# Performance work log

Measured on AMD Instinct MI355X. Metric: run time of the kernel, lower is better.

Reference implementation:

```python
import jax, jax.numpy as jnp
import numpy as np

D_MODEL = 1024
HEADS = 16
HEAD_DIM = D_MODEL // HEADS


def setup_inputs() -> dict:
    key = jax.random.key(0)
    k1, k2 = jax.random.split(key)
    x = jax.random.normal(k1, (2, 2048, D_MODEL), dtype=jnp.float32)
    # nn.Linear(d_model, 3*d_model, bias=False): weight shape [3*d_model, d_model]
    W_qkv = jax.random.normal(k2, (3 * D_MODEL, D_MODEL), dtype=jnp.float32) * (D_MODEL ** -0.5)
    return {"x": x, "W_qkv": W_qkv}


def reference(x, W_qkv):
    b, t, c = x.shape
    qkv = jnp.einsum('btc,fc->btf', x, W_qkv)  # [b, t, 3c]
    q, k, v = jnp.split(qkv, 3, axis=-1)
    # [b, heads, t, head_dim]
    q = q.reshape(b, t, HEADS, HEAD_DIM).transpose(0, 2, 1, 3)
    k = k.reshape(b, t, HEADS, HEAD_DIM).transpose(0, 2, 1, 3)
    v = v.reshape(b, t, HEADS, HEAD_DIM).transpose(0, 2, 1, 3)
    scores = jnp.einsum('bhqd,bhkd->bhqk', q, k) * (HEAD_DIM ** -0.5)
    causal = jnp.tril(jnp.ones((t, t), dtype=bool))  # [t, t]
    scores = jnp.where(causal[None, None, :, :], scores, -jnp.inf)
    weights = jax.nn.softmax(scores, axis=-1)
    out = jnp.einsum('bhqk,bhkd->bhqd', weights, v)
    return out.transpose(0, 2, 1, 3).reshape(b, t, c)
```

## Files before the change

kernel.cpp:

```cpp
#include <hip/hip_runtime.h>
#include <hip/hip_bf16.h>
#include <stdint.h>

#define D_MODEL 1024
#define TOKENS  2048
#define HEADS   16
#define HDIM    64
#define NQKV    3072
#define MROWS   4096
#define SCALE   0.18033688011112042f

typedef __attribute__((ext_vector_type(4)))  float f32x4;
typedef __attribute__((ext_vector_type(16))) float f32x16;
typedef __attribute__((ext_vector_type(8)))  short bf16x8;

__device__ __forceinline__ unsigned short f2bf(float f) {
  union { float f; unsigned u; } v; v.f = f;
  unsigned u = v.u + 0x7FFFu + ((v.u >> 16) & 1u);
  return (unsigned short)(u >> 16);
}
__device__ __forceinline__ float bf2f(unsigned short b) {
  union { unsigned u; float f; } v; v.u = ((unsigned)b) << 16;
  return v.f;
}
__device__ __forceinline__ unsigned cvt_pk_bf16(float lo, float hi) {
  unsigned r;
  asm("v_cvt_pk_bf16_f32 %0, %1, %2" : "=v"(r) : "v"(lo), "v"(hi));
  return r;
}
__device__ __forceinline__ float xchg32(float v) {
  return __shfl_xor(v, 32);
}
__device__ __forceinline__ bf16x8 pfrag8(const float* g) {
  union { uint4 u; bf16x8 v; } r;
  r.u.x = cvt_pk_bf16(g[0], g[1]);
  r.u.y = cvt_pk_bf16(g[2], g[3]);
  r.u.z = cvt_pk_bf16(g[4], g[5]);
  r.u.w = cvt_pk_bf16(g[6], g[7]);
  return r.v;
}
__device__ __forceinline__ float max32t(const f32x16& a, const f32x16& b) {
  float t[16];
#pragma unroll
  for (int r = 0; r < 16; ++r) t[r] = fmaxf(a[r], b[r]);
#pragma unroll
  for (int s = 8; s > 0; s >>= 1)
#pragma unroll
    for (int r = 0; r < s; ++r) t[r] = fmaxf(t[r], t[r + s]);
  return t[0];
}
__device__ __forceinline__ float sum32t(const float* a, const float* b) {
  float t[16];
#pragma unroll
  for (int r = 0; r < 16; ++r) t[r] = a[r] + b[r];
#pragma unroll
  for (int s = 8; s > 0; s >>= 1)
#pragma unroll
    for (int r = 0; r < s; ++r) t[r] = t[r] + t[r + s];
  return t[0];
}

#define GLOAD16(g, l)                                                          \
  __builtin_amdgcn_global_load_lds(                                            \
      (const __attribute__((address_space(1))) unsigned int*)(g),              \
      (__attribute__((address_space(3))) unsigned int*)(l), 16, 0, 0)

__global__ __launch_bounds__(256) void cvt_bf16(const float* __restrict__ X,
                                                const float* __restrict__ W,
                                                unsigned short* __restrict__ Xb,
                                                unsigned short* __restrict__ Wb) {
  const size_t NX = (size_t)MROWS * D_MODEL;
  size_t i = ((size_t)blockIdx.x * 256 + threadIdx.x) * 8;
  const float* src; unsigned short* dst; size_t off;
  if (i < NX) { src = X; dst = Xb; off = i; }
  else        { src = W; dst = Wb; off = i - NX; }
  float4 a = ((const float4*)(src + off))[0];
  float4 b = ((const float4*)(src + off))[1];
  union { unsigned short s[8]; uint4 v; } u;
  u.s[0] = f2bf(a.x); u.s[1] = f2bf(a.y); u.s[2] = f2bf(a.z); u.s[3] = f2bf(a.w);
  u.s[4] = f2bf(b.x); u.s[5] = f2bf(b.y); u.s[6] = f2bf(b.z); u.s[7] = f2bf(b.w);
  *(uint4*)(dst + off) = u.v;
}

__global__ __launch_bounds__(512, 1) void gemm8(const unsigned short* __restrict__ A,
                                                const unsigned short* __restrict__ B,
                                                unsigned short* __restrict__ C) {
  __shared__ unsigned short sA[2][2][128][64];
  __shared__ unsigned short sB[2][2][128][64];

  const int tid  = threadIdx.x;
  const int lane = tid & 63;
  const int wave = tid >> 6;
  const int wr   = wave >> 2;
  const int wc   = wave & 3;
  const int l15  = lane & 15;
  const int lg   = lane >> 4;

  const int bm = blockIdx.x;
  const int bn = blockIdx.y;

  f32x4 acc[8][4];
#pragma unroll
  for (int i = 0; i < 8; ++i)
#pragma unroll
    for (int j = 0; j < 4; ++j)
#pragma unroll
      for (int r = 0; r < 4; ++r) acc[i][j][r] = 0.f;

  const int srow = tid >> 3;
  const int scb  = (tid & 7) * 16;
  const int ssce = (scb ^ ((srow & 7) << 4)) >> 1;

  const unsigned short* Ag = A + (size_t)(bm * 256) * D_MODEL;
  const unsigned short* Bg = B + (size_t)(bn * 256) * D_MODEL;

#define STG_A(buf, hf, t)                                                      \
  { GLOAD16(Ag + (size_t)((hf) * 128 + srow) * D_MODEL + (t) * 64 + ssce,      \
            (char*)&sA[buf][hf][0][0] + srow * 128 + scb);                     \
    GLOAD16(Ag + (size_t)((hf) * 128 + 64 + srow) * D_MODEL + (t) * 64 + ssce, \
            (char*)&sA[buf][hf][0][0] + 8192 + srow * 128 + scb); }
#define STG_B(buf, hf, t)                                                      \
  { GLOAD16(Bg + (size_t)((hf) * 128 + srow) * D_MODEL + (t) * 64 + ssce,      \
            (char*)&sB[buf][hf][0][0] + srow * 128 + scb);                     \
    GLOAD16(Bg + (size_t)((hf) * 128 + 64 + srow) * D_MODEL + (t) * 64 + ssce, \
            (char*)&sB[buf][hf][0][0] + 8192 + srow * 128 + scb); }

  const char* aBse[2] = { (const char*)&sA[0][wr][0][0], (const char*)&sA[1][wr][0][0] };
  const char* bBse[2] = { (const char*)&sB[0][wc >> 1][0][0], (const char*)&sB[1][wc >> 1][0][0] };
  const int swzl = (l15 & 7) << 4;
  const int cbs0 = (lg * 16) ^ swzl;
  const int cbs1 = (64 + lg * 16) ^ swzl;
  const int arow = l15 * 128;
  const int brow = ((wc & 1) * 64 + l15) * 128;

  bf16x8 aF[4][2];

#define DO_PHASE(qm, qn, buf, LD_A, STAGE_STMT, DO_VM)                         \
  {                                                                            \
    if (LD_A) {                                                                \
      _Pragma("unroll")                                                        \
      for (int i = 0; i < 4; ++i) {                                            \
        aF[i][0] = *(const bf16x8*)(aBse[buf] + ((qm)*4 + i) * 2048 + arow + cbs0); \
        aF[i][1] = *(const bf16x8*)(aBse[buf] + ((qm)*4 + i) * 2048 + arow + cbs1); \
      }                                                                        \
    }                                                                          \
    bf16x8 b_[2][2];                                                           \
    _Pragma("unroll")                                                          \
    for (int n = 0; n < 2; ++n) {                                              \
      b_[n][0] = *(const bf16x8*)(bBse[buf] + ((qn)*2 + n) * 2048 + brow + cbs0); \
      b_[n][1] = *(const bf16x8*)(bBse[buf] + ((qn)*2 + n) * 2048 + brow + cbs1); \
    }                                                                          \
    STAGE_STMT;                                                                \
    if (DO_VM) asm volatile("s_waitcnt vmcnt(2)" ::: "memory");                \
    __builtin_amdgcn_s_barrier();                                              \
    asm volatile("s_waitcnt lgkmcnt(0)" ::: "memory");                         \
    __builtin_amdgcn_sched_barrier(0);                                         \
    __builtin_amdgcn_s_setprio(1);                                             \
    _Pragma("unroll")                                                          \
    for (int ks = 0; ks < 2; ++ks)                                             \
      _Pragma("unroll")                                                        \
      for (int i = 0; i < 4; ++i)                                              \
        _Pragma("unroll")                                                      \
        for (int n = 0; n < 2; ++n)                                            \
          acc[(qm)*4 + i][(qn)*2 + n] = __builtin_amdgcn_mfma_f32_16x16x32_bf16( \
              aF[i][ks], b_[n][ks], acc[(qm)*4 + i][(qn)*2 + n], 0, 0, 0);     \
    __builtin_amdgcn_s_setprio(0);                                             \
    __builtin_amdgcn_s_barrier();                                              \
  }

  STG_A(0, 0, 0);
  STG_B(0, 0, 0);
  STG_A(0, 1, 0);
  STG_B(0, 1, 0);
  STG_B(1, 0, 1);
  asm volatile("s_waitcnt vmcnt(2)" ::: "memory");
  __builtin_amdgcn_s_barrier();

#pragma unroll 1
  for (int j = 0; j < 8; ++j) {
    const int t1 = 2 * j + 1;
    const int t2 = 2 * j + 2;
    const int t3 = 2 * j + 3;
    DO_PHASE(0, 0, 0, 1, { STG_A(1, 0, t1); }, 0);
    DO_PHASE(0, 1, 0, 0, { STG_A(1, 1, t1); }, 0);
    DO_PHASE(1, 0, 0, 1, { STG_B(1, 1, t1); }, 0);
    DO_PHASE(1, 1, 0, 0, { if (t2 < 16) STG_B(0, 0, t2); }, 1);
    DO_PHASE(0, 0, 1, 1, { if (t2 < 16) STG_A(0, 0, t2); }, 0);
    DO_PHASE(0, 1, 1, 0, { if (t2 < 16) STG_A(0, 1, t2); }, 0);
    DO_PHASE(1, 0, 1, 1, { if (t2 < 16) STG_B(0, 1, t2); }, 0);
    DO_PHASE(1, 1, 1, 0, { if (t3 < 16) STG_B(1, 0, t3); }, 1);
  }

  const int orow0 = bm * 256 + wr * 128 + lg * 4;
  const int ocol0 = bn * 256 + wc * 64 + l15;
#pragma unroll
  for (int mi = 0; mi < 8; ++mi)
#pragma unroll
    for (int ni = 0; ni < 4; ++ni)
#pragma unroll
      for (int r = 0; r < 4; ++r)
        C[(size_t)(orow0 + mi * 16 + r) * NQKV + ocol0 + ni * 16] = f2bf(acc[mi][ni][r]);
#undef STG_A
#undef STG_B
#undef DO_PHASE
}

__global__ __launch_bounds__(256) void qkv_gemm(const float* __restrict__ X,
                                                const float* __restrict__ W,
                                                unsigned short* __restrict__ QKV) {
  __shared__ unsigned short sA[128 * 32];
  __shared__ unsigned short sB[128 * 32];
  const int tid  = threadIdx.x;
  const int lane = tid & 63;
  const int wave = tid >> 6;
  const int wr = wave >> 1, wc = wave & 1;
  const int row0 = blockIdx.x * 128;
  const int col0 = blockIdx.y * 128;

  f32x4 acc[4][4];
#pragma unroll
  for (int i = 0; i < 4; ++i)
#pragma unroll
    for (int j = 0; j < 4; ++j)
#pragma unroll
      for (int r = 0; r < 4; ++r) acc[i][j][r] = 0.f;

  const int srow = tid >> 1;
  const int scol = (tid & 1) * 16;
  union U16 { unsigned short s[8]; uint4 v; };

#pragma unroll 1
  for (int k0 = 0; k0 < D_MODEL; k0 += 32) {
    {
      const float* ga = X + (size_t)(row0 + srow) * D_MODEL + k0 + scol;
      const float* gb = W + (size_t)(col0 + srow) * D_MODEL + k0 + scol;
      float va[16], vb[16];
#pragma unroll
      for (int i = 0; i < 4; ++i) {
        float4 t = ((const float4*)ga)[i];
        va[4*i+0] = t.x; va[4*i+1] = t.y; va[4*i+2] = t.z; va[4*i+3] = t.w;
        float4 u = ((const float4*)gb)[i];
        vb[4*i+0] = u.x; vb[4*i+1] = u.y; vb[4*i+2] = u.z; vb[4*i+3] = u.w;
      }
      U16 ua0, ua1, ub0, ub1;
#pragma unroll
      for (int e = 0; e < 8; ++e) {
        ua0.s[e] = f2bf(va[e]);   ua1.s[e] = f2bf(va[8 + e]);
        ub0.s[e] = f2bf(vb[e]);   ub1.s[e] = f2bf(vb[8 + e]);
      }
      *(uint4*)&sA[srow * 32 + scol + 0] = ua0.v;
      *(uint4*)&sA[srow * 32 + scol + 8] = ua1.v;
      *(uint4*)&sB[srow * 32 + scol + 0] = ub0.v;
      *(uint4*)&sB[srow * 32 + scol + 8] = ub1.v;
    }
    __syncthreads();

    const int lrow = lane & 15;
    const int lk   = (lane >> 4) * 8;
    bf16x8 av[4], bv[4];
#pragma unroll
    for (int i = 0; i < 4; ++i)
      av[i] = *(const bf16x8*)&sA[(wr * 64 + i * 16 + lrow) * 32 + lk];
#pragma unroll
    for (int j = 0; j < 4; ++j)
      bv[j] = *(const bf16x8*)&sB[(wc * 64 + j * 16 + lrow) * 32 + lk];
#pragma unroll
    for (int i = 0; i < 4; ++i)
#pragma unroll
      for (int j = 0; j < 4; ++j)
        acc[i][j] = __builtin_amdgcn_mfma_f32_16x16x32_bf16(av[i], bv[j], acc[i][j], 0, 0, 0);
    __syncthreads();
  }

  const int orow = row0 + wr * 64 + (lane >> 4) * 4;
  const int ocol = col0 + wc * 64 + (lane & 15);
#pragma unroll
  for (int i = 0; i < 4; ++i)
#pragma unroll
    for (int j = 0; j < 4; ++j)
#pragma unroll
      for (int r = 0; r < 4; ++r)
        QKV[(size_t)(orow + i * 16 + r) * NQKV + ocol + j * 16] = f2bf(acc[i][j][r]);
}

__global__ __launch_bounds__(256, 2) void attn10(const unsigned short* __restrict__ QKV,
                                                 float* __restrict__ Out) {
  __shared__ unsigned short sK [2][2][64 * 64];
  __shared__ unsigned short sVt[2][2][64 * 64];

  const int tid  = threadIdx.x;
  const int lane = tid & 63;
  const int wave = tid >> 6;
  const int l31  = lane & 31;
  const int hi   = lane >> 5;

  const int x = blockIdx.x;
  int bh, u;
  if (x < 256) { bh = x & 31; u = x >> 5; }
  else         { const int x2 = x - 256; bh = x2 & 31; u = 15 - (x2 >> 5); }

  const int b = bh >> 4, h = bh & 15;
  const int q0w  = u * 128 + wave * 32;
  const int qcol = q0w + l31;

  const unsigned short* Qbase = QKV + (size_t)(b * TOKENS) * NQKV + h * HDIM;
  const unsigned short* Kbase = Qbase + D_MODEL;
  const unsigned short* Vbase = Kbase + D_MODEL;

  bf16x8 qf[4];
  {
    const unsigned short* qrow = Qbase + (size_t)qcol * NQKV + hi * 8;
    union { unsigned short us[8]; bf16x8 v; ushort4 q[2]; } t;
#pragma unroll
    for (int dk = 0; dk < 4; ++dk) {
      t.q[0] = ((const ushort4*)(qrow + dk * 16))[0];
      t.q[1] = ((const ushort4*)(qrow + dk * 16))[1];
#pragma unroll
      for (int e = 0; e < 8; ++e) t.us[e] = f2bf(bf2f(t.us[e]) * SCALE);
      qf[dk] = t.v;
    }
  }

  f32x16 o0, o1;
#pragma unroll
  for (int r = 0; r < 16; ++r) { o0[r] = 0.f; o1[r] = 0.f; }
  float m = -1e30f, ll = 0.f;

  const int vk0 = (tid & 15) * 4;
  const int vd0 = (tid >> 4) * 4;
  ushort4 va0, va1, va2, va3, vb0, vb1, vb2, vb3;

  const int lane16 = lane * 16;

#define KGLOAD(kt, buf, s)                                                     \
  {                                                                            \
    _Pragma("unroll")                                                          \
    for (int g = 0; g < 2; ++g) {                                              \
      const int base = g * 4096 + wave * 1024;                                 \
      const int d = base + lane16;                                             \
      const int row = d >> 7;                                                  \
      const int grow = (row & 51) | ((row & 4) << 1) | ((row & 8) >> 1);       \
      const int cb = (d & 127) ^ ((row & 7) << 4);                             \
      GLOAD16(Kbase + (size_t)((kt) * 64 + grow) * NQKV + (cb >> 1),           \
              (char*)&sK[buf][s][0] + base + lane16);                          \
    }                                                                          \
  }

#define VLOAD2(pp)                                                             \
  {                                                                            \
    const unsigned short* vsA = Vbase + (size_t)((2*(pp)) * 64 + vk0) * NQKV + vd0;   \
    va0 = *(const ushort4*)(vsA);                                              \
    va1 = *(const ushort4*)(vsA + NQKV);                                       \
    va2 = *(const ushort4*)(vsA + 2 * NQKV);                                   \
    va3 = *(const ushort4*)(vsA + 3 * NQKV);                                   \
    const unsigned short* vsB = Vbase + (size_t)((2*(pp)+1) * 64 + vk0) * NQKV + vd0; \
    vb0 = *(const ushort4*)(vsB);                                              \
    vb1 = *(const ushort4*)(vsB + NQKV);                                       \
    vb2 = *(const ushort4*)(vsB + 2 * NQKV);                                   \
    vb3 = *(const ushort4*)(vsB + 3 * NQKV);                                   \
  }

#define VWRITE1(buf, s, t0, t1, t2, t3)                                        \
  {                                                                            \
    ushort4 c0, c1, c2, c3;                                                    \
    c0.x = t0.x; c0.y = t1.x; c0.z = t2.x; c0.w = t3.x;                        \
    c1.x = t0.y; c1.y = t1.y; c1.z = t2.y; c1.w = t3.y;                        \
    c2.x = t0.z; c2.y = t1.z; c2.z = t2.z; c2.w = t3.z;                        \
    c3.x = t0.w; c3.y = t1.w; c3.z = t2.w; c3.w = t3.w;                        \
    char* dV = (char*)&sVt[buf][s][0];                                         \
    _Pragma("unroll")                                                          \
    for (int e = 0; e < 4; ++e) {                                              \
      const int dim = vd0 + e;                                                 \
      const int o2 = (dim * 128 + vk0 * 2) ^ ((dim & 7) << 4);                 \
      ushort4 cc = (e == 0) ? c0 : (e == 1) ? c1 : (e == 2) ? c2 : c3;         \
      *(ushort4*)(dV + o2) = cc;                                               \
    }                                                                          \
  }

#define QKT(cK, rowbase, st)                                                   \
  {                                                                            \
    _Pragma("unroll")                                                          \
    for (int dk = 0; dk < 4; ++dk) {                                           \
      const int row = (rowbase);                                               \
      bf16x8 kf = *(const bf16x8*)((cK) + ((row * 128 + hi * 16 + dk * 32) ^ ((row & 7) << 4))); \
      st = __builtin_amdgcn_mfma_f32_32x32x16_bf16(kf, qf[dk], st, 0, 0, 0);   \
    }                                                                          \
  }

#define PV4(cV, bpX, bpY, koff)                                                \
  {                                                                            \
    const int r0 = l31, r1 = l31 + 32;                                         \
    bf16x8 vf;                                                                 \
    vf = *(const bf16x8*)((cV) + ((r0 * 128 + hi * 16 + (koff)) ^ ((r0 & 7) << 4)));      \
    o0 = __builtin_amdgcn_mfma_f32_32x32x16_bf16(vf, bpX, o0, 0, 0, 0);        \
    vf = *(const bf16x8*)((cV) + ((r1 * 128 + hi * 16 + (koff)) ^ ((r1 & 7) << 4)));      \
    o1 = __builtin_amdgcn_mfma_f32_32x32x16_bf16(vf, bpX, o1, 0, 0, 0);        \
    vf = *(const bf16x8*)((cV) + ((r0 * 128 + hi * 16 + (koff) + 32) ^ ((r0 & 7) << 4))); \
    o0 = __builtin_amdgcn_mfma_f32_32x32x16_bf16(vf, bpY, o0, 0, 0, 0);        \
    vf = *(const bf16x8*)((cV) + ((r1 * 128 + hi * 16 + (koff) + 32) ^ ((r1 & 7) << 4))); \
    o1 = __builtin_amdgcn_mfma_f32_32x32x16_bf16(vf, bpY, o1, 0, 0, 0);        \
  }

#define MUPDATE(mx)                                                            \
  {                                                                            \
    if (!__all((mx) - m <= 8.f)) {                                             \
      float mw = fmaxf((mx), xchg32(mx));                                      \
      const float mnew = fmaxf(m, mw);                                         \
      const float corr = exp2f(m - mnew);                                      \
      m = mnew;                                                                \
      ll *= corr;                                                              \
      _Pragma("unroll")                                                        \
      for (int r = 0; r < 16; ++r) { o0[r] *= corr; o1[r] *= corr; }           \
    }                                                                          \
  }

  KGLOAD(0, 0, 0);
  KGLOAD(1, 0, 1);
  VLOAD2(0);
  VWRITE1(0, 0, va0, va1, va2, va3);
  VWRITE1(0, 1, vb0, vb1, vb2, vb3);
  __syncthreads();

#pragma unroll 1
  for (int p = 0; p < u; ++p) {
    const int cur = p & 1;
    KGLOAD(2 * (p + 1),     cur ^ 1, 0);
    KGLOAD(2 * (p + 1) + 1, cur ^ 1, 1);
    VLOAD2(p + 1);

    const char* cKA = (const char*)&sK[cur][0][0];
    const char* cKB = (const char*)&sK[cur][1][0];
    const char* cVA = (const char*)&sVt[cur][0][0];
    const char* cVB = (const char*)&sVt[cur][1][0];

    f32x16 sA0, sA1, sB0, sB1;
#pragma unroll
    for (int r = 0; r < 16; ++r) { sA0[r] = 0.f; sA1[r] = 0.f; sB0[r] = 0.f; sB1[r] = 0.f; }

    QKT(cKA, l31,      sA0);
    QKT(cKA, l31 + 32, sA1);
    QKT(cKB, l31,      sB0);
    QKT(cKB, l31 + 32, sB1);

    {
      float mx = max32t(sA0, sA1);
      MUPDATE(mx);
      float pA0[16], pA1[16];
#pragma unroll
      for (int r = 0; r < 16; ++r) { pA0[r] = exp2f(sA0[r] - m); pA1[r] = exp2f(sA1[r] - m); }
      ll += sum32t(pA0, pA1);
      bf16x8 a0 = pfrag8(&pA0[0]), a1 = pfrag8(&pA0[8]);
      bf16x8 a2 = pfrag8(&pA1[0]), a3 = pfrag8(&pA1[8]);
      PV4(cVA, a0, a1, 0);
      PV4(cVA, a2, a3, 64);
    }

    {
      float mx = max32t(sB0, sB1);
      MUPDATE(mx);
      float pB0[16], pB1[16];
#pragma unroll
      for (int r = 0; r < 16; ++r) { pB0[r] = exp2f(sB0[r] - m); pB1[r] = exp2f(sB1[r] - m); }
      ll += sum32t(pB0, pB1);
      bf16x8 b0 = pfrag8(&pB0[0]), b1 = pfrag8(&pB0[8]);
      bf16x8 b2 = pfrag8(&pB1[0]), b3 = pfrag8(&pB1[8]);
      PV4(cVB, b0, b1, 0);
      PV4(cVB, b2, b3, 64);
    }

    VWRITE1(cur ^ 1, 0, va0, va1, va2, va3);
    VWRITE1(cur ^ 1, 1, vb0, vb1, vb2, vb3);
    __syncthreads();
  }

  {
    const int cur = u & 1;
    const char* cK[2] = { (const char*)&sK[cur][0][0], (const char*)&sK[cur][1][0] };
    const char* cV[2] = { (const char*)&sVt[cur][0][0], (const char*)&sVt[cur][1][0] };
    const int nsub = (wave >= 2) ? 2 : 1;
#pragma unroll 1
    for (int s = 0; s < nsub; ++s) {
      const int kbase = u * 128 + s * 64;
      const bool diag  = (wave >= 2) ? (s == 1) : true;
      const bool do_hi = diag ? ((wave & 1) == 1) : true;

      f32x16 st0, st1;
#pragma unroll
      for (int r = 0; r < 16; ++r) { st0[r] = 0.f; st1[r] = 0.f; }

      QKT(cK[s], l31, st0);
      if (do_hi) QKT(cK[s], l31 + 32, st1);

      if (diag) {
#pragma unroll
        for (int r = 0; r < 16; ++r) {
          const int key0 = kbase + (r & 7) + ((r & 8) << 1) + 8 * hi;
          if (key0 > qcol) st0[r] = -1e30f;
          if (do_hi && key0 + 32 > qcol) st1[r] = -1e30f;
        }
      }

      float mx = do_hi ? max32t(st0, st1) : max32t(st0, st0);
      MUPDATE(mx);

      float p0[16], p1[16];
#pragma unroll
      for (int r = 0; r < 16; ++r) p0[r] = exp2f(st0[r] - m);
      if (do_hi) {
#pragma unroll
        for (int r = 0; r < 16; ++r) p1[r] = exp2f(st1[r] - m);
        ll += sum32t(p0, p1);
      } else {
        float z[16];
#pragma unroll
        for (int r = 0; r < 16; ++r) z[r] = 0.f;
        ll += sum32t(p0, z);
      }

      bf16x8 c0 = pfrag8(&p0[0]), c1 = pfrag8(&p0[8]);
      PV4(cV[s], c0, c1, 0);
      if (do_hi) {
        bf16x8 c2 = pfrag8(&p1[0]), c3 = pfrag8(&p1[8]);
        PV4(cV[s], c2, c3, 64);
      }
    }
  }

  {
    const float lfull = ll + xchg32(ll);
    const float inv = 1.f / lfull;
    float* orow = Out + (size_t)(b * TOKENS + qcol) * D_MODEL + h * HDIM;
#pragma unroll
    for (int g = 0; g < 4; ++g) {
      float4 w0, w1;
      w0.x = o0[4*g+0] * inv; w0.y = o0[4*g+1] * inv;
      w0.z = o0[4*g+2] * inv; w0.w = o0[4*g+3] * inv;
      w1.x = o1[4*g+0] * inv; w1.y = o1[4*g+1] * inv;
      w1.z = o1[4*g+2] * inv; w1.w = o1[4*g+3] * inv;
      *(float4*)(orow + 8 * g + 4 * hi)      = w0;
      *(float4*)(orow + 8 * g + 4 * hi + 32) = w1;
    }
  }
#undef KGLOAD
#undef VLOAD2
#undef VWRITE1
#undef QKT
#undef PV4
#undef MUPDATE
}

extern "C" void kernel_launch(void* const* d_in, const int* in_sizes, int n_in,
                              void* d_out, int out_size, void* d_ws, size_t ws_size,
                              hipStream_t stream) {
  const float* X = (const float*)d_in[0];
  const float* W = (const float*)d_in[1];
  float* Out = (float*)d_out;
  unsigned short* QKV = (unsigned short*)d_ws;

  const size_t QKV_E = (size_t)MROWS * NQKV;
  const size_t XB_E  = (size_t)MROWS * D_MODEL;
  const size_t WB_E  = (size_t)NQKV * D_MODEL;
  const size_t need_bf16 = (QKV_E + XB_E + WB_E) * 2;

  if (ws_size >= need_bf16) {
    unsigned short* Xb = QKV + QKV_E;
    unsigned short* Wb = Xb + XB_E;
    cvt_bf16<<<(XB_E + WB_E) / (256 * 8), 256, 0, stream>>>(X, W, Xb, Wb);
    gemm8<<<dim3(MROWS / 256, NQKV / 256), 512, 0, stream>>>(Xb, Wb, QKV);
  } else {
    qkv_gemm<<<dim3(MROWS / 128, NQKV / 128), 256, 0, stream>>>(X, W, QKV);
  }

  attn10<<<512, 256, 0, stream>>>(QKV, Out);
}
```

Measured before the change: 98.29 us.

## Split PV accumulators into independent chains and remap block-to-tile order

Measured after the change: 115.5 us. 1.18x slower.

```diff
diff --git a/kernel.cpp b/kernel.cpp
--- a/kernel.cpp
+++ b/kernel.cpp
@@ -283,7 +283,7 @@
         QKV[(size_t)(orow + i * 16 + r) * NQKV + ocol + j * 16] = f2bf(acc[i][j][r]);
 }
 
-__global__ __launch_bounds__(256, 2) void attn10(const unsigned short* __restrict__ QKV,
+__global__ __launch_bounds__(256, 2) void attn11(const unsigned short* __restrict__ QKV,
                                                  float* __restrict__ Out) {
   __shared__ unsigned short sK [2][2][64 * 64];
   __shared__ unsigned short sVt[2][2][64 * 64];
@@ -295,17 +295,19 @@
   const int hi   = lane >> 5;
 
   const int x = blockIdx.x;
-  int bh, u;
-  if (x < 256) { bh = x & 31; u = x >> 5; }
-  else         { const int x2 = x - 256; bh = x2 & 31; u = 15 - (x2 >> 5); }
-
-  const int b = bh >> 4, h = bh & 15;
+  const int i256 = x & 255;
+  const int u  = i256 >> 4;
+  const int h  = i256 & 15;
+  const int b  = x >> 8;
+  const int bh = (b << 4) | h;
+
   const int q0w  = u * 128 + wave * 32;
   const int qcol = q0w + l31;
 
   const unsigned short* Qbase = QKV + (size_t)(b * TOKENS) * NQKV + h * HDIM;
   const unsigned short* Kbase = Qbase + D_MODEL;
   const unsigned short* Vbase = Kbase + D_MODEL;
+  (void)bh;
 
   bf16x8 qf[4];
   {
@@ -321,9 +323,9 @@
     }
   }
 
-  f32x16 o0, o1;
-#pragma unroll
-  for (int r = 0; r < 16; ++r) { o0[r] = 0.f; o1[r] = 0.f; }
+  f32x16 o0a, o0b, o1a, o1b;
+#pragma unroll
+  for (int r = 0; r < 16; ++r) { o0a[r] = 0.f; o0b[r] = 0.f; o1a[r] = 0.f; o1b[r] = 0.f; }
   float m = -1e30f, ll = 0.f;
 
   const int vk0 = (tid & 15) * 4;
@@ -392,13 +394,13 @@
     const int r0 = l31, r1 = l31 + 32;                                         \
     bf16x8 vf;                                                                 \
     vf = *(const bf16x8*)((cV) + ((r0 * 128 + hi * 16 + (koff)) ^ ((r0 & 7) << 4)));      \
-    o0 = __builtin_amdgcn_mfma_f32_32x32x16_bf16(vf, bpX, o0, 0, 0, 0);        \
+    o0a = __builtin_amdgcn_mfma_f32_32x32x16_bf16(vf, bpX, o0a, 0, 0, 0);      \
     vf = *(const bf16x8*)((cV) + ((r1 * 128 + hi * 16 + (koff)) ^ ((r1 & 7) << 4)));      \
-    o1 = __builtin_amdgcn_mfma_f32_32x32x16_bf16(vf, bpX, o1, 0, 0, 0);        \
+    o1a = __builtin_amdgcn_mfma_f32_32x32x16_bf16(vf, bpX, o1a, 0, 0, 0);      \
     vf = *(const bf16x8*)((cV) + ((r0 * 128 + hi * 16 + (koff) + 32) ^ ((r0 & 7) << 4))); \
-    o0 = __builtin_amdgcn_mfma_f32_32x32x16_bf16(vf, bpY, o0, 0, 0, 0);        \
+    o0b = __builtin_amdgcn_mfma_f32_32x32x16_bf16(vf, bpY, o0b, 0, 0, 0);      \
     vf = *(const bf16x8*)((cV) + ((r1 * 128 + hi * 16 + (koff) + 32) ^ ((r1 & 7) << 4))); \
-    o1 = __builtin_amdgcn_mfma_f32_32x32x16_bf16(vf, bpY, o1, 0, 0, 0);        \
+    o1b = __builtin_amdgcn_mfma_f32_32x32x16_bf16(vf, bpY, o1b, 0, 0, 0);      \
   }
 
 #define MUPDATE(mx)                                                            \
@@ -410,7 +412,9 @@
       m = mnew;                                                                \
       ll *= corr;                                                              \
       _Pragma("unroll")                                                        \
-      for (int r = 0; r < 16; ++r) { o0[r] *= corr; o1[r] *= corr; }           \
+      for (int r = 0; r < 16; ++r) {                                           \
+        o0a[r] *= corr; o0b[r] *= corr; o1a[r] *= corr; o1b[r] *= corr;        \
+      }                                                                        \
     }                                                                          \
   }
 
@@ -533,10 +537,14 @@
 #pragma unroll
     for (int g = 0; g < 4; ++g) {
       float4 w0, w1;
-      w0.x = o0[4*g+0] * inv; w0.y = o0[4*g+1] * inv;
-      w0.z = o0[4*g+2] * inv; w0.w = o0[4*g+3] * inv;
-      w1.x = o1[4*g+0] * inv; w1.y = o1[4*g+1] * inv;
-      w1.z = o1[4*g+2] * inv; w1.w = o1[4*g+3] * inv;
+      w0.x = (o0a[4*g+0] + o0b[4*g+0]) * inv;
+      w0.y = (o0a[4*g+1] + o0b[4*g+1]) * inv;
+      w0.z = (o0a[4*g+2] + o0b[4*g+2]) * inv;
+      w0.w = (o0a[4*g+3] + o0b[4*g+3]) * inv;
+      w1.x = (o1a[4*g+0] + o1b[4*g+0]) * inv;
+      w1.y = (o1a[4*g+1] + o1b[4*g+1]) * inv;
+      w1.z = (o1a[4*g+2] + o1b[4*g+2]) * inv;
+      w1.w = (o1a[4*g+3] + o1b[4*g+3]) * inv;
       *(float4*)(orow + 8 * g + 4 * hi)      = w0;
       *(float4*)(orow + 8 * g + 4 * hi + 32) = w1;
     }
@@ -571,5 +579,5 @@
     qkv_gemm<<<dim3(MROWS / 128, NQKV / 128), 256, 0, stream>>>(X, W, QKV);
   }
 
-  attn10<<<512, 256, 0, stream>>>(QKV, Out);
-}
+  attn11<<<512, 256, 0, stream>>>(QKV, Out);
+}
```
